# Kernel optimization log

Hardware: AMD Instinct MI355X
Metric: run time of the kernel (lower is better)

The kernel has to match this reference:

```python
import jax, jax.numpy as jnp
import numpy as np

N_NODES = 50000


def _gcn_layer(x, src, dst, W, b, n_nodes):
    # PyG GCNConv: h = x @ W, add self-loops, sym-normalized scatter-add, + bias
    h = x @ W  # [N, Dout]
    loop = jnp.arange(n_nodes, dtype=src.dtype)
    src2 = jnp.concatenate([src, loop])
    dst2 = jnp.concatenate([dst, loop])
    ones = jnp.ones(src2.shape[0], dtype=x.dtype)
    deg = jax.ops.segment_sum(ones, dst2, num_segments=n_nodes)  # in-degree w/ self-loops
    dinv = jnp.where(deg > 0, jax.lax.rsqrt(deg), 0.0)
    norm = dinv[src2] * dinv[dst2]  # [E+N]
    msg = h[src2] * norm[:, None]   # gather + scale
    out = jax.ops.segment_sum(msg, dst2, num_segments=n_nodes)  # scatter-add
    return out + b


def setup_inputs() -> dict:
    key = jax.random.key(0)
    k1, k2, k3, k4 = jax.random.split(key, 4)
    x = jax.random.normal(k1, (N_NODES, 128), dtype=jnp.float32)
    edge_index = jax.random.randint(k2, (2, 500000), 0, N_NODES, dtype=jnp.int64)
    W1 = jax.random.normal(k3, (128, 128), dtype=jnp.float32) * (1.0 / np.sqrt(128))
    b1 = jnp.zeros((128,), dtype=jnp.float32)
    W2 = jax.random.normal(k4, (128, 64), dtype=jnp.float32) * (1.0 / np.sqrt(128))
    b2 = jnp.zeros((64,), dtype=jnp.float32)
    return {"x": x, "edge_index": edge_index, "W1": W1, "b1": b1, "W2": W2, "b2": b2}


def reference(x, edge_index, W1, b1, W2, b2):
    src, dst = edge_index[0], edge_index[1]
    n = x.shape[0]
    h = _gcn_layer(x, src, dst, W1, b1, n)
    h = jax.nn.relu(h)
    out = _gcn_layer(h, src, dst, W2, b2, n)
    return out
```

## Files before the change

kernel.cpp:

```cpp
#include <hip/hip_runtime.h>
#include <hip/hip_bf16.h>
#include <cstddef>


typedef __attribute__((ext_vector_type(8))) short short8;
typedef __attribute__((ext_vector_type(4))) float f32x4;

__device__ inline unsigned short f2bf(float f) {
    __hip_bfloat16 b = __float2bfloat16(f);
    return *reinterpret_cast<unsigned short*>(&b);
}
__device__ inline float bf2f_lo(unsigned int u) {
    unsigned int v = u << 16;
    return *reinterpret_cast<float*>(&v);
}
__device__ inline float bf2f_hi(unsigned int u) {
    unsigned int v = u & 0xffff0000u;
    return *reinterpret_cast<float*>(&v);
}

__global__ __launch_bounds__(256) void count_kernel(const int* __restrict__ dst, int E,
                                                    int* __restrict__ deg) {
    int i = blockIdx.x * blockDim.x + threadIdx.x;
    if (i < E) atomicAdd(&deg[dst[i]], 1);
}

__global__ __launch_bounds__(256) void scanA_kernel(const int* __restrict__ deg, int n,
                                                    int* __restrict__ bsums) {
    int tid = threadIdx.x;
    int lane = tid & 63;
    int wid = tid >> 6;
    int i = blockIdx.x * 1024 + tid * 4;
    int v0 = (i + 0 < n) ? deg[i + 0] : 0;
    int v1 = (i + 1 < n) ? deg[i + 1] : 0;
    int v2 = (i + 2 < n) ? deg[i + 2] : 0;
    int v3 = (i + 3 < n) ? deg[i + 3] : 0;
    int s = v0 + v1 + v2 + v3;
    #pragma unroll
    for (int off = 32; off > 0; off >>= 1) s += __shfl_down(s, off, 64);
    __shared__ int ws[4];
    if (lane == 0) ws[wid] = s;
    __syncthreads();
    if (tid == 0) bsums[blockIdx.x] = ws[0] + ws[1] + ws[2] + ws[3];
}

__global__ __launch_bounds__(64) void scanB_kernel(int* __restrict__ bsums, int nb,
                                                   int* __restrict__ totp) {
    int lane = threadIdx.x;
    int v = (lane < nb) ? bsums[lane] : 0;
    int x = v;
    #pragma unroll
    for (int off = 1; off < 64; off <<= 1) {
        int y = __shfl_up(x, off, 64);
        if (lane >= off) x += y;
    }
    if (lane < nb) bsums[lane] = x - v;
    if (lane == 63) *totp = x;
}

__global__ __launch_bounds__(256) void scanC_kernel(const int* __restrict__ deg, int n,
                                                    const int* __restrict__ bsums,
                                                    int* __restrict__ offs,
                                                    int* __restrict__ cur,
                                                    float* __restrict__ dinv) {
    int tid = threadIdx.x;
    int lane = tid & 63;
    int wid = tid >> 6;
    int carry = bsums[blockIdx.x];
    int i = blockIdx.x * 1024 + tid * 4;
    int v0 = (i + 0 < n) ? deg[i + 0] : 0;
    int v1 = (i + 1 < n) ? deg[i + 1] : 0;
    int v2 = (i + 2 < n) ? deg[i + 2] : 0;
    int v3 = (i + 3 < n) ? deg[i + 3] : 0;
    int t = v0 + v1 + v2 + v3;
    int x = t;
    #pragma unroll
    for (int off = 1; off < 64; off <<= 1) {
        int y = __shfl_up(x, off, 64);
        if (lane >= off) x += y;
    }
    __shared__ int ws[4];
    if (lane == 63) ws[wid] = x;
    __syncthreads();
    int wprefix = 0;
    #pragma unroll
    for (int w = 0; w < 4; w++) wprefix += (w < wid) ? ws[w] : 0;
    int e0 = carry + wprefix + x - t;
    int e1 = e0 + v0, e2 = e1 + v1, e3 = e2 + v2;
    if (i + 0 < n) { offs[i + 0] = e0; cur[i + 0] = e0; dinv[i + 0] = rsqrtf((float)(v0 + 1)); }
    if (i + 1 < n) { offs[i + 1] = e1; cur[i + 1] = e1; dinv[i + 1] = rsqrtf((float)(v1 + 1)); }
    if (i + 2 < n) { offs[i + 2] = e2; cur[i + 2] = e2; dinv[i + 2] = rsqrtf((float)(v2 + 1)); }
    if (i + 3 < n) { offs[i + 3] = e3; cur[i + 3] = e3; dinv[i + 3] = rsqrtf((float)(v3 + 1)); }
}

__global__ __launch_bounds__(256) void fill_kernel(const int* __restrict__ src,
                                                   const int* __restrict__ dst, int E,
                                                   int* __restrict__ cur,
                                                   const float* __restrict__ dinv,
                                                   unsigned int* __restrict__ csr) {
    int i = blockIdx.x * blockDim.x + threadIdx.x;
    if (i < E) {
        int s = src[i];
        int d = dst[i];
        int p = atomicAdd(&cur[d], 1);
        float w = dinv[s] * dinv[d];
        csr[p] = (unsigned int)s | ((unsigned int)f2bf(w) << 16);
    }
}

__global__ __launch_bounds__(256) void wt_frag_kernel(const float* __restrict__ W1,
                                                      const float* __restrict__ W2,
                                                      unsigned short* __restrict__ W1f,
                                                      unsigned short* __restrict__ W2f) {
    int idx = blockIdx.x * 256 + threadIdx.x;
    const float* W;
    unsigned short* Wf;
    int n, oct, N;
    if (idx < 2048) { W = W1; Wf = W1f; N = 128; n = idx >> 4; oct = idx & 15; }
    else if (idx < 3072) { W = W2; Wf = W2f; N = 64; int i2 = idx - 2048; n = i2 >> 4; oct = i2 & 15; }
    else return;
    int k0 = oct * 8;
    int ks = k0 >> 5, quad = (k0 >> 3) & 3, ntg = n >> 4;
    short8 v;
    #pragma unroll
    for (int j = 0; j < 8; j++) v[j] = (short)f2bf(W[(k0 + j) * N + n]);
    int off = (((ntg * 4 + ks) * 64) + (n & 15) + 16 * quad) * 8;
    *(short8*)(Wf + off) = v;
}

__global__ __launch_bounds__(256) void gemm1_kernel(const float* __restrict__ A,
                                                    const unsigned short* __restrict__ Bf,
                                                    unsigned short* __restrict__ C,
                                                    int M) {
    constexpr int K = 128, BN = 128;
    __shared__ unsigned short As[64 * K];

    int tid = threadIdx.x;
    int lane = tid & 63;
    int w = tid >> 6;
    int row0 = blockIdx.x * 64;

    short8 bfr[2][4];
    #pragma unroll
    for (int nl = 0; nl < 2; nl++)
        #pragma unroll
        for (int ks = 0; ks < 4; ks++)
            bfr[nl][ks] = *(const short8*)(Bf + ((((w * 2 + nl) * 4 + ks) * 64) + lane) * 8);

    #pragma unroll
    for (int it = 0; it < 8; it++) {
        int idx = it * 256 + tid;
        int row = idx >> 5, kq = idx & 31;
        int k0 = kq * 4;
        int ks = k0 >> 5, quad = (k0 >> 3) & 3, j0 = k0 & 7, mt = row >> 4;
        ushort4 o = make_ushort4(0, 0, 0, 0);
        int gr = row0 + row;
        if (gr < M) {
            float4 a = *(const float4*)(A + (size_t)gr * K + k0);
            o.x = f2bf(a.x); o.y = f2bf(a.y); o.z = f2bf(a.z); o.w = f2bf(a.w);
        }
        int off = (((mt * 4 + ks) * 64) + (row & 15) + 16 * quad) * 8 + j0;
        *(ushort4*)(As + off) = o;
    }
    __syncthreads();

    f32x4 acc[4][2];
    #pragma unroll
    for (int mt = 0; mt < 4; mt++)
        #pragma unroll
        for (int nl = 0; nl < 2; nl++) acc[mt][nl] = (f32x4){0.f, 0.f, 0.f, 0.f};

    #pragma unroll
    for (int ks = 0; ks < 4; ks++) {
        short8 af[4];
        #pragma unroll
        for (int mt = 0; mt < 4; mt++)
            af[mt] = *(const short8*)(As + (((mt * 4 + ks) * 64) + lane) * 8);
        #pragma unroll
        for (int mt = 0; mt < 4; mt++)
            #pragma unroll
            for (int nl = 0; nl < 2; nl++)
                acc[mt][nl] = __builtin_amdgcn_mfma_f32_16x16x32_bf16(
                    af[mt], bfr[nl][ks], acc[mt][nl], 0, 0, 0);
    }

    int col16 = lane & 15;
    int rowq = lane >> 4;
    #pragma unroll
    for (int mt = 0; mt < 4; mt++) {
        #pragma unroll
        for (int nl = 0; nl < 2; nl++) {
            int gc = (w * 2 + nl) * 16 + col16;
            #pragma unroll
            for (int r = 0; r < 4; r++) {
                int gr = row0 + mt * 16 + rowq * 4 + r;
                if (gr < M) C[(size_t)gr * BN + gc] = f2bf(acc[mt][nl][r]);
            }
        }
    }
}

__global__ __launch_bounds__(256) void aggmm_kernel(const unsigned short* __restrict__ h1,
                                                    const int* __restrict__ offs,
                                                    const unsigned int* __restrict__ csr,
                                                    const float* __restrict__ dinv,
                                                    const float* __restrict__ b1,
                                                    const unsigned short* __restrict__ W2f,
                                                    unsigned short* __restrict__ h2,
                                                    int n) {
    __shared__ unsigned short As[4 * 64 * 8];

    int tid = threadIdx.x;
    int t = tid & 63;
    int w = tid >> 6;
    int p = t >> 5;
    int t5 = t & 31;
    int nodebase = blockIdx.x * 16;

    short8 bw[4];
    #pragma unroll
    for (int ks = 0; ks < 4; ks++)
        bw[ks] = *(const short8*)(W2f + (((w * 4 + ks) * 64) + t) * 8);

    float4 bias = *(const float4*)(b1 + t5 * 4);

    #pragma unroll
    for (int i = 0; i < 4; i++) {
        int row16 = w * 4 + i;
        int node = nodebase + row16;
        float a0 = 0.f, a1 = 0.f, a2 = 0.f, a3 = 0.f;
        if (node < n) {
            float di = dinv[node];
            float sw = di * di;
            if (p == 0) {
                uint2 su = *(const uint2*)(h1 + (size_t)node * 128 + t5 * 4);
                a0 = bf2f_lo(su.x) * sw; a1 = bf2f_hi(su.x) * sw;
                a2 = bf2f_lo(su.y) * sw; a3 = bf2f_hi(su.y) * sw;
            }
            int e0 = offs[node];
            int e1 = offs[node + 1];
            int iters = (e1 - e0 + 7) >> 3;
            for (int it = 0; it < iters; it++) {
                int eb = e0 + it * 8;
                #pragma unroll
                for (int j = 0; j < 4; j++) {
                    int ee = eb + j * 2 + p;
                    int ec = min(ee, e1 - 1);
                    unsigned int pk = csr[ec];
                    float wgt = (ee < e1) ? bf2f_hi(pk) : 0.f;
                    int s = pk & 0xffff;
                    uint2 hu = *(const uint2*)(h1 + (size_t)s * 128 + t5 * 4);
                    a0 += bf2f_lo(hu.x) * wgt; a1 += bf2f_hi(hu.x) * wgt;
                    a2 += bf2f_lo(hu.y) * wgt; a3 += bf2f_hi(hu.y) * wgt;
                }
            }
        }
        a0 += __shfl_xor(a0, 32, 64);
        a1 += __shfl_xor(a1, 32, 64);
        a2 += __shfl_xor(a2, 32, 64);
        a3 += __shfl_xor(a3, 32, 64);
        if (p == 0) {
            if (node < n) {
                a0 = fmaxf(a0 + bias.x, 0.f);
                a1 = fmaxf(a1 + bias.y, 0.f);
                a2 = fmaxf(a2 + bias.z, 0.f);
                a3 = fmaxf(a3 + bias.w, 0.f);
            }
            int k0 = t5 * 4;
            int ks = k0 >> 5, quad = (k0 >> 3) & 3, j0 = k0 & 7;
            ushort4 pk4 = make_ushort4(f2bf(a0), f2bf(a1), f2bf(a2), f2bf(a3));
            *(ushort4*)(As + ((ks * 64) + row16 + 16 * quad) * 8 + j0) = pk4;
        }
    }
    __syncthreads();

    f32x4 acc = (f32x4){0.f, 0.f, 0.f, 0.f};
    #pragma unroll
    for (int ks = 0; ks < 4; ks++) {
        short8 af = *(const short8*)(As + ((ks * 64) + t) * 8);
        acc = __builtin_amdgcn_mfma_f32_16x16x32_bf16(af, bw[ks], acc, 0, 0, 0);
    }

    int col = w * 16 + (t & 15);
    int rowq = t >> 4;
    #pragma unroll
    for (int r = 0; r < 4; r++) {
        int gr = nodebase + rowq * 4 + r;
        if (gr < n) h2[(size_t)gr * 64 + col] = f2bf(acc[r]);
    }
}

__global__ __launch_bounds__(256) void aggout_kernel(const unsigned short* __restrict__ h2,
                                                     const int* __restrict__ offs,
                                                     const unsigned int* __restrict__ csr,
                                                     const float* __restrict__ dinv,
                                                     const float* __restrict__ b2,
                                                     float* __restrict__ out, int n) {
    int tid = threadIdx.x;
    int t = tid & 63;
    int w = tid >> 6;
    int node = blockIdx.x * 4 + w;
    if (node >= n) return;
    int p = t >> 4;
    int t4 = t & 15;

    float a0 = 0.f, a1 = 0.f, a2 = 0.f, a3 = 0.f;
    float di = dinv[node];
    float sw = di * di;
    if (p == 0) {
        uint2 su = *(const uint2*)(h2 + (size_t)node * 64 + t4 * 4);
        a0 = bf2f_lo(su.x) * sw; a1 = bf2f_hi(su.x) * sw;
        a2 = bf2f_lo(su.y) * sw; a3 = bf2f_hi(su.y) * sw;
    }

    int e0 = offs[node];
    int e1 = offs[node + 1];
    int iters = (e1 - e0 + 7) >> 3;
    for (int it = 0; it < iters; it++) {
        int eb = e0 + it * 8;
        #pragma unroll
        for (int j = 0; j < 2; j++) {
            int ee = eb + j * 4 + p;
            int ec = min(ee, e1 - 1);
            unsigned int pk = csr[ec];
            float wgt = (ee < e1) ? bf2f_hi(pk) : 0.f;
            int s = pk & 0xffff;
            uint2 hu = *(const uint2*)(h2 + (size_t)s * 64 + t4 * 4);
            a0 += bf2f_lo(hu.x) * wgt; a1 += bf2f_hi(hu.x) * wgt;
            a2 += bf2f_lo(hu.y) * wgt; a3 += bf2f_hi(hu.y) * wgt;
        }
    }
    a0 += __shfl_xor(a0, 16, 64); a1 += __shfl_xor(a1, 16, 64);
    a2 += __shfl_xor(a2, 16, 64); a3 += __shfl_xor(a3, 16, 64);
    a0 += __shfl_xor(a0, 32, 64); a1 += __shfl_xor(a1, 32, 64);
    a2 += __shfl_xor(a2, 32, 64); a3 += __shfl_xor(a3, 32, 64);
    if (p == 0) {
        float4 bb = *(const float4*)(b2 + t4 * 4);
        *(float4*)(out + (size_t)node * 64 + t4 * 4) =
            make_float4(a0 + bb.x, a1 + bb.y, a2 + bb.z, a3 + bb.w);
    }
}

extern "C" void kernel_launch(void* const* d_in, const int* in_sizes, int n_in,
                              void* d_out, int out_size, void* d_ws, size_t ws_size,
                              hipStream_t stream) {
    const float* x  = (const float*)d_in[0];
    const int*   ei = (const int*)d_in[1];
    const float* W1 = (const float*)d_in[2];
    const float* b1 = (const float*)d_in[3];
    const float* W2 = (const float*)d_in[4];
    const float* b2 = (const float*)d_in[5];

    const int N = in_sizes[0] / 128;
    const int E = in_sizes[1] / 2;
    const int* src = ei;
    const int* dst = ei + E;

    char* p = (char*)d_ws;
    auto alloc = [&](size_t bytes) {
        char* r = p;
        p += (bytes + 255) & ~(size_t)255;
        return r;
    };
    int*   degi  = (int*)  alloc((size_t)N * 4);
    float* dinv  = (float*)alloc((size_t)N * 4);
    int*   offs  = (int*)  alloc((size_t)(N + 1) * 4);
    int*   cur   = (int*)  alloc((size_t)N * 4);
    int*   bsums = (int*)  alloc((size_t)64 * 4);
    unsigned int*   csr  = (unsigned int*)alloc((size_t)E * 4);
    unsigned short* W1f  = (unsigned short*)alloc((size_t)128 * 128 * 2);
    unsigned short* W2f  = (unsigned short*)alloc((size_t)64 * 128 * 2);
    unsigned short* h1   = (unsigned short*)alloc((size_t)N * 128 * 2);
    unsigned short* h2   = (unsigned short*)alloc((size_t)N * 64 * 2);
    float* out = (float*)d_out;

    const int NB = (N + 1023) / 1024;

    wt_frag_kernel<<<12, 256, 0, stream>>>(W1, W2, W1f, W2f);
    hipMemsetAsync(degi, 0, (size_t)N * 4, stream);
    count_kernel<<<(E + 255) / 256, 256, 0, stream>>>(dst, E, degi);
    scanA_kernel<<<NB, 256, 0, stream>>>(degi, N, bsums);
    scanB_kernel<<<1, 64, 0, stream>>>(bsums, NB, offs + N);
    scanC_kernel<<<NB, 256, 0, stream>>>(degi, N, bsums, offs, cur, dinv);
    fill_kernel<<<(E + 255) / 256, 256, 0, stream>>>(src, dst, E, cur, dinv, csr);

    gemm1_kernel<<<(N + 63) / 64, 256, 0, stream>>>(x, W1f, h1, N);
    aggmm_kernel<<<(N + 15) / 16, 256, 0, stream>>>(h1, offs, csr, dinv, b1, W2f, h2, N);
    aggout_kernel<<<(N + 3) / 4, 256, 0, stream>>>(h2, offs, csr, dinv, b2, out, N);
}
```

Measured before the change: 197.2 us.

## Fuse graph build and first GEMM into one persistent kernel with flag sync

```diff
diff --git a/kernel.cpp b/kernel.cpp
--- a/kernel.cpp
+++ b/kernel.cpp
@@ -5,6 +5,7 @@
 
 typedef __attribute__((ext_vector_type(8))) short short8;
 typedef __attribute__((ext_vector_type(4))) float f32x4;
+typedef unsigned long long u64;
 
 __device__ inline unsigned short f2bf(float f) {
     __hip_bfloat16 b = __float2bfloat16(f);
@@ -19,184 +20,226 @@
     return *reinterpret_cast<float*>(&v);
 }
 
-__global__ __launch_bounds__(256) void count_kernel(const int* __restrict__ dst, int E,
-                                                    int* __restrict__ deg) {
-    int i = blockIdx.x * blockDim.x + threadIdx.x;
-    if (i < E) atomicAdd(&deg[dst[i]], 1);
-}
-
-__global__ __launch_bounds__(256) void scanA_kernel(const int* __restrict__ deg, int n,
-                                                    int* __restrict__ bsums) {
+__device__ inline u64 ld_acq64(u64* p) {
+    return __hip_atomic_load(p, __ATOMIC_ACQUIRE, __HIP_MEMORY_SCOPE_AGENT);
+}
+__device__ inline void st_rel64(u64* p, u64 v) {
+    __hip_atomic_store(p, v, __ATOMIC_RELEASE, __HIP_MEMORY_SCOPE_AGENT);
+}
+__device__ inline int ld_acq32(int* p) {
+    return __hip_atomic_load(p, __ATOMIC_ACQUIRE, __HIP_MEMORY_SCOPE_AGENT);
+}
+
+__global__ __launch_bounds__(256) void init_kernel(const float* __restrict__ W1,
+                                                   const float* __restrict__ W2,
+                                                   unsigned short* __restrict__ W1f,
+                                                   unsigned short* __restrict__ W2f,
+                                                   int* __restrict__ deg,
+                                                   u64* __restrict__ lb,
+                                                   int* __restrict__ flags, int N) {
+    int idx = blockIdx.x * 256 + threadIdx.x;
+    if (idx < N) deg[idx] = 0;
+    if (idx < 64) lb[idx] = 0;
+    if (idx < 4) flags[idx] = 0;
+    if (idx < 3072) {
+        const float* W;
+        unsigned short* Wf;
+        int n, oct, Nc;
+        if (idx < 2048) { W = W1; Wf = W1f; Nc = 128; n = idx >> 4; oct = idx & 15; }
+        else { W = W2; Wf = W2f; Nc = 64; int i2 = idx - 2048; n = i2 >> 4; oct = i2 & 15; }
+        int k0 = oct * 8;
+        int ks = k0 >> 5, quad = (k0 >> 3) & 3, ntg = n >> 4;
+        short8 v;
+        #pragma unroll
+        for (int j = 0; j < 8; j++) v[j] = (short)f2bf(W[(k0 + j) * Nc + n]);
+        int off = (((ntg * 4 + ks) * 64) + (n & 15) + 16 * quad) * 8;
+        *(short8*)(Wf + off) = v;
+    }
+}
+
+#define MEGA_CB 256
+
+__global__ __launch_bounds__(256) void mega_kernel(
+    const float* __restrict__ x, const unsigned short* __restrict__ W1f,
+    unsigned short* __restrict__ h1,
+    const int* __restrict__ src, const int* __restrict__ dst, int E,
+    int* __restrict__ deg, int N,
+    u64* __restrict__ lb, int* __restrict__ offs, int* __restrict__ cur,
+    float* __restrict__ dinv, unsigned int* __restrict__ csr,
+    int* __restrict__ flags) {
+
+    const int GB = (N + 63) / 64;
+    const int CB = MEGA_CB;
+    const int SB = (N + 1023) / 1024;
+    int b = blockIdx.x;
     int tid = threadIdx.x;
+
+    __shared__ unsigned short As[64 * 128];
+    __shared__ int ws[4];
+    __shared__ int s_prefix;
+
+    if (b < GB) {
+        constexpr int K = 128, BN = 128;
+        int lane = tid & 63;
+        int w = tid >> 6;
+        int row0 = b * 64;
+
+        short8 bfr[2][4];
+        #pragma unroll
+        for (int nl = 0; nl < 2; nl++)
+            #pragma unroll
+            for (int ks = 0; ks < 4; ks++)
+                bfr[nl][ks] = *(const short8*)(W1f + ((((w * 2 + nl) * 4 + ks) * 64) + lane) * 8);
+
+        #pragma unroll
+        for (int it = 0; it < 8; it++) {
+            int idx = it * 256 + tid;
+            int row = idx >> 5, kq = idx & 31;
+            int k0 = kq * 4;
+            int ks = k0 >> 5, quad = (k0 >> 3) & 3, j0 = k0 & 7, mt = row >> 4;
+            ushort4 o = make_ushort4(0, 0, 0, 0);
+            int gr = row0 + row;
+            if (gr < N) {
+                float4 a = *(const float4*)(x + (size_t)gr * K + k0);
+                o.x = f2bf(a.x); o.y = f2bf(a.y); o.z = f2bf(a.z); o.w = f2bf(a.w);
+            }
+            int off = (((mt * 4 + ks) * 64) + (row & 15) + 16 * quad) * 8 + j0;
+            *(ushort4*)(As + off) = o;
+        }
+        __syncthreads();
+
+        f32x4 acc[4][2];
+        #pragma unroll
+        for (int mt = 0; mt < 4; mt++)
+            #pragma unroll
+            for (int nl = 0; nl < 2; nl++) acc[mt][nl] = (f32x4){0.f, 0.f, 0.f, 0.f};
+
+        #pragma unroll
+        for (int ks = 0; ks < 4; ks++) {
+            short8 af[4];
+            #pragma unroll
+            for (int mt = 0; mt < 4; mt++)
+                af[mt] = *(const short8*)(As + (((mt * 4 + ks) * 64) + lane) * 8);
+            #pragma unroll
+            for (int mt = 0; mt < 4; mt++)
+                #pragma unroll
+                for (int nl = 0; nl < 2; nl++)
+                    acc[mt][nl] = __builtin_amdgcn_mfma_f32_16x16x32_bf16(
+                        af[mt], bfr[nl][ks], acc[mt][nl], 0, 0, 0);
+        }
+
+        int col16 = lane & 15;
+        int rowq = lane >> 4;
+        #pragma unroll
+        for (int mt = 0; mt < 4; mt++) {
+            #pragma unroll
+            for (int nl = 0; nl < 2; nl++) {
+                int gc = (w * 2 + nl) * 16 + col16;
+                #pragma unroll
+                for (int r = 0; r < 4; r++) {
+                    int gr = row0 + mt * 16 + rowq * 4 + r;
+                    if (gr < N) h1[(size_t)gr * BN + gc] = f2bf(acc[mt][nl][r]);
+                }
+            }
+        }
+        return;
+    }
+
+    if (b < GB + CB) {
+        int cb = b - GB;
+        for (int i = cb * 256 + tid; i < E; i += CB * 256)
+            atomicAdd(&deg[dst[i]], 1);
+        __syncthreads();
+        if (tid == 0) {
+            __threadfence_system();
+            atomicAdd(&flags[0], 1);
+            while (ld_acq32(&flags[1]) < SB) __builtin_amdgcn_s_sleep(2);
+            __threadfence_system();
+        }
+        __syncthreads();
+        for (int i = cb * 256 + tid; i < E; i += CB * 256) {
+            int s = src[i];
+            int d = dst[i];
+            int p = atomicAdd(&cur[d], 1);
+            float w = rsqrtf((float)((deg[s] + 1) * (deg[d] + 1)));
+            csr[p] = (unsigned int)s | ((unsigned int)f2bf(w) << 16);
+        }
+        return;
+    }
+
+    int sb = b - GB - CB;
+    if (tid == 0) {
+        while (ld_acq32(&flags[0]) < CB) __builtin_amdgcn_s_sleep(2);
+        __threadfence_system();
+    }
+    __syncthreads();
+
     int lane = tid & 63;
-    int wid = tid >> 6;
-    int i = blockIdx.x * 1024 + tid * 4;
-    int v0 = (i + 0 < n) ? deg[i + 0] : 0;
-    int v1 = (i + 1 < n) ? deg[i + 1] : 0;
-    int v2 = (i + 2 < n) ? deg[i + 2] : 0;
-    int v3 = (i + 3 < n) ? deg[i + 3] : 0;
-    int s = v0 + v1 + v2 + v3;
-    #pragma unroll
-    for (int off = 32; off > 0; off >>= 1) s += __shfl_down(s, off, 64);
-    __shared__ int ws[4];
-    if (lane == 0) ws[wid] = s;
-    __syncthreads();
-    if (tid == 0) bsums[blockIdx.x] = ws[0] + ws[1] + ws[2] + ws[3];
-}
-
-__global__ __launch_bounds__(64) void scanB_kernel(int* __restrict__ bsums, int nb,
-                                                   int* __restrict__ totp) {
-    int lane = threadIdx.x;
-    int v = (lane < nb) ? bsums[lane] : 0;
-    int x = v;
+    int wv = tid >> 6;
+    int i = sb * 1024 + tid * 4;
+    int v0 = (i + 0 < N) ? deg[i + 0] : 0;
+    int v1 = (i + 1 < N) ? deg[i + 1] : 0;
+    int v2 = (i + 2 < N) ? deg[i + 2] : 0;
+    int v3 = (i + 3 < N) ? deg[i + 3] : 0;
+    int tsum = v0 + v1 + v2 + v3;
+    int xs = tsum;
     #pragma unroll
     for (int off = 1; off < 64; off <<= 1) {
-        int y = __shfl_up(x, off, 64);
-        if (lane >= off) x += y;
-    }
-    if (lane < nb) bsums[lane] = x - v;
-    if (lane == 63) *totp = x;
-}
-
-__global__ __launch_bounds__(256) void scanC_kernel(const int* __restrict__ deg, int n,
-                                                    const int* __restrict__ bsums,
-                                                    int* __restrict__ offs,
-                                                    int* __restrict__ cur,
-                                                    float* __restrict__ dinv) {
-    int tid = threadIdx.x;
-    int lane = tid & 63;
-    int wid = tid >> 6;
-    int carry = bsums[blockIdx.x];
-    int i = blockIdx.x * 1024 + tid * 4;
-    int v0 = (i + 0 < n) ? deg[i + 0] : 0;
-    int v1 = (i + 1 < n) ? deg[i + 1] : 0;
-    int v2 = (i + 2 < n) ? deg[i + 2] : 0;
-    int v3 = (i + 3 < n) ? deg[i + 3] : 0;
-    int t = v0 + v1 + v2 + v3;
-    int x = t;
-    #pragma unroll
-    for (int off = 1; off < 64; off <<= 1) {
-        int y = __shfl_up(x, off, 64);
-        if (lane >= off) x += y;
-    }
-    __shared__ int ws[4];
-    if (lane == 63) ws[wid] = x;
+        int y = __shfl_up(xs, off, 64);
+        if (lane >= off) xs += y;
+    }
+    if (lane == 63) ws[wv] = xs;
     __syncthreads();
     int wprefix = 0;
     #pragma unroll
-    for (int w = 0; w < 4; w++) wprefix += (w < wid) ? ws[w] : 0;
-    int e0 = carry + wprefix + x - t;
+    for (int w2 = 0; w2 < 4; w2++) wprefix += (w2 < wv) ? ws[w2] : 0;
+    int chunk_total = ws[0] + ws[1] + ws[2] + ws[3];
+
+    if (tid == 0) {
+        st_rel64(&lb[sb], ((u64)(unsigned)chunk_total << 2) | 1ull);
+        int prefix = 0;
+        for (int pred = sb - 1; pred >= 0; --pred) {
+            u64 v;
+            do {
+                v = ld_acq64(&lb[pred]);
+                if ((v & 3) == 0) __builtin_amdgcn_s_sleep(1);
+            } while ((v & 3) == 0);
+            prefix += (int)(unsigned)(v >> 2);
+            if ((v & 3) == 2) break;
+        }
+        st_rel64(&lb[sb], ((u64)(unsigned)(prefix + chunk_total) << 2) | 2ull);
+        s_prefix = prefix;
+    }
+    __syncthreads();
+
+    int carry = s_prefix;
+    int e0 = carry + wprefix + xs - tsum;
     int e1 = e0 + v0, e2 = e1 + v1, e3 = e2 + v2;
-    if (i + 0 < n) { offs[i + 0] = e0; cur[i + 0] = e0; dinv[i + 0] = rsqrtf((float)(v0 + 1)); }
-    if (i + 1 < n) { offs[i + 1] = e1; cur[i + 1] = e1; dinv[i + 1] = rsqrtf((float)(v1 + 1)); }
-    if (i + 2 < n) { offs[i + 2] = e2; cur[i + 2] = e2; dinv[i + 2] = rsqrtf((float)(v2 + 1)); }
-    if (i + 3 < n) { offs[i + 3] = e3; cur[i + 3] = e3; dinv[i + 3] = rsqrtf((float)(v3 + 1)); }
-}
-
-__global__ __launch_bounds__(256) void fill_kernel(const int* __restrict__ src,
-                                                   const int* __restrict__ dst, int E,
-                                                   int* __restrict__ cur,
-                                                   const float* __restrict__ dinv,
-                                                   unsigned int* __restrict__ csr) {
-    int i = blockIdx.x * blockDim.x + threadIdx.x;
-    if (i < E) {
-        int s = src[i];
-        int d = dst[i];
-        int p = atomicAdd(&cur[d], 1);
-        float w = dinv[s] * dinv[d];
-        csr[p] = (unsigned int)s | ((unsigned int)f2bf(w) << 16);
-    }
-}
-
-__global__ __launch_bounds__(256) void wt_frag_kernel(const float* __restrict__ W1,
-                                                      const float* __restrict__ W2,
-                                                      unsigned short* __restrict__ W1f,
-                                                      unsigned short* __restrict__ W2f) {
-    int idx = blockIdx.x * 256 + threadIdx.x;
-    const float* W;
-    unsigned short* Wf;
-    int n, oct, N;
-    if (idx < 2048) { W = W1; Wf = W1f; N = 128; n = idx >> 4; oct = idx & 15; }
-    else if (idx < 3072) { W = W2; Wf = W2f; N = 64; int i2 = idx - 2048; n = i2 >> 4; oct = i2 & 15; }
-    else return;
-    int k0 = oct * 8;
-    int ks = k0 >> 5, quad = (k0 >> 3) & 3, ntg = n >> 4;
-    short8 v;
-    #pragma unroll
-    for (int j = 0; j < 8; j++) v[j] = (short)f2bf(W[(k0 + j) * N + n]);
-    int off = (((ntg * 4 + ks) * 64) + (n & 15) + 16 * quad) * 8;
-    *(short8*)(Wf + off) = v;
-}
-
-__global__ __launch_bounds__(256) void gemm1_kernel(const float* __restrict__ A,
-                                                    const unsigned short* __restrict__ Bf,
-                                                    unsigned short* __restrict__ C,
-                                                    int M) {
-    constexpr int K = 128, BN = 128;
-    __shared__ unsigned short As[64 * K];
-
-    int tid = threadIdx.x;
-    int lane = tid & 63;
-    int w = tid >> 6;
-    int row0 = blockIdx.x * 64;
-
-    short8 bfr[2][4];
-    #pragma unroll
-    for (int nl = 0; nl < 2; nl++)
-        #pragma unroll
-        for (int ks = 0; ks < 4; ks++)
-            bfr[nl][ks] = *(const short8*)(Bf + ((((w * 2 + nl) * 4 + ks) * 64) + lane) * 8);
-
-    #pragma unroll
-    for (int it = 0; it < 8; it++) {
-        int idx = it * 256 + tid;
-        int row = idx >> 5, kq = idx & 31;
-        int k0 = kq * 4;
-        int ks = k0 >> 5, quad = (k0 >> 3) & 3, j0 = k0 & 7, mt = row >> 4;
-        ushort4 o = make_ushort4(0, 0, 0, 0);
-        int gr = row0 + row;
-        if (gr < M) {
-            float4 a = *(const float4*)(A + (size_t)gr * K + k0);
-            o.x = f2bf(a.x); o.y = f2bf(a.y); o.z = f2bf(a.z); o.w = f2bf(a.w);
-        }
-        int off = (((mt * 4 + ks) * 64) + (row & 15) + 16 * quad) * 8 + j0;
-        *(ushort4*)(As + off) = o;
-    }
+    if (i + 0 < N) {
+        offs[i + 0] = e0;
+        __hip_atomic_store(&cur[i + 0], e0, __ATOMIC_RELAXED, __HIP_MEMORY_SCOPE_AGENT);
+        dinv[i + 0] = rsqrtf((float)(v0 + 1));
+    }
+    if (i + 1 < N) {
+        offs[i + 1] = e1;
+        __hip_atomic_store(&cur[i + 1], e1, __ATOMIC_RELAXED, __HIP_MEMORY_SCOPE_AGENT);
+        dinv[i + 1] = rsqrtf((float)(v1 + 1));
+    }
+    if (i + 2 < N) {
+        offs[i + 2] = e2;
+        __hip_atomic_store(&cur[i + 2], e2, __ATOMIC_RELAXED, __HIP_MEMORY_SCOPE_AGENT);
+        dinv[i + 2] = rsqrtf((float)(v2 + 1));
+    }
+    if (i + 3 < N) {
+        offs[i + 3] = e3;
+        __hip_atomic_store(&cur[i + 3], e3, __ATOMIC_RELAXED, __HIP_MEMORY_SCOPE_AGENT);
+        dinv[i + 3] = rsqrtf((float)(v3 + 1));
+    }
+    if (sb == SB - 1 && tid == 0) offs[N] = carry + chunk_total;
     __syncthreads();
-
-    f32x4 acc[4][2];
-    #pragma unroll
-    for (int mt = 0; mt < 4; mt++)
-        #pragma unroll
-        for (int nl = 0; nl < 2; nl++) acc[mt][nl] = (f32x4){0.f, 0.f, 0.f, 0.f};
-
-    #pragma unroll
-    for (int ks = 0; ks < 4; ks++) {
-        short8 af[4];
-        #pragma unroll
-        for (int mt = 0; mt < 4; mt++)
-            af[mt] = *(const short8*)(As + (((mt * 4 + ks) * 64) + lane) * 8);
-        #pragma unroll
-        for (int mt = 0; mt < 4; mt++)
-            #pragma unroll
-            for (int nl = 0; nl < 2; nl++)
-                acc[mt][nl] = __builtin_amdgcn_mfma_f32_16x16x32_bf16(
-                    af[mt], bfr[nl][ks], acc[mt][nl], 0, 0, 0);
-    }
-
-    int col16 = lane & 15;
-    int rowq = lane >> 4;
-    #pragma unroll
-    for (int mt = 0; mt < 4; mt++) {
-        #pragma unroll
-        for (int nl = 0; nl < 2; nl++) {
-            int gc = (w * 2 + nl) * 16 + col16;
-            #pragma unroll
-            for (int r = 0; r < 4; r++) {
-                int gr = row0 + mt * 16 + rowq * 4 + r;
-                if (gr < M) C[(size_t)gr * BN + gc] = f2bf(acc[mt][nl][r]);
-            }
-        }
+    if (tid == 0) {
+        __threadfence_system();
+        atomicAdd(&flags[1], 1);
     }
 }
 
@@ -366,7 +409,8 @@
     float* dinv  = (float*)alloc((size_t)N * 4);
     int*   offs  = (int*)  alloc((size_t)(N + 1) * 4);
     int*   cur   = (int*)  alloc((size_t)N * 4);
-    int*   bsums = (int*)  alloc((size_t)64 * 4);
+    u64*   lb    = (u64*)  alloc((size_t)64 * 8);
+    int*   flags = (int*)  alloc((size_t)4 * 4);
     unsigned int*   csr  = (unsigned int*)alloc((size_t)E * 4);
     unsigned short* W1f  = (unsigned short*)alloc((size_t)128 * 128 * 2);
     unsigned short* W2f  = (unsigned short*)alloc((size_t)64 * 128 * 2);
@@ -374,17 +418,13 @@
     unsigned short* h2   = (unsigned short*)alloc((size_t)N * 64 * 2);
     float* out = (float*)d_out;
 
-    const int NB = (N + 1023) / 1024;
-
-    wt_frag_kernel<<<12, 256, 0, stream>>>(W1, W2, W1f, W2f);
-    hipMemsetAsync(degi, 0, (size_t)N * 4, stream);
-    count_kernel<<<(E + 255) / 256, 256, 0, stream>>>(dst, E, degi);
-    scanA_kernel<<<NB, 256, 0, stream>>>(degi, N, bsums);
-    scanB_kernel<<<1, 64, 0, stream>>>(bsums, NB, offs + N);
-    scanC_kernel<<<NB, 256, 0, stream>>>(degi, N, bsums, offs, cur, dinv);
-    fill_kernel<<<(E + 255) / 256, 256, 0, stream>>>(src, dst, E, cur, dinv, csr);
-
-    gemm1_kernel<<<(N + 63) / 64, 256, 0, stream>>>(x, W1f, h1, N);
+    const int GB = (N + 63) / 64;
+    const int SB = (N + 1023) / 1024;
+    const int MEGA = GB + MEGA_CB + SB;
+
+    init_kernel<<<(N + 255) / 256, 256, 0, stream>>>(W1, W2, W1f, W2f, degi, lb, flags, N);
+    mega_kernel<<<MEGA, 256, 0, stream>>>(x, W1f, h1, src, dst, E, degi, N,
+                                          lb, offs, cur, dinv, csr, flags);
     aggmm_kernel<<<(N + 15) / 16, 256, 0, stream>>>(h1, offs, csr, dinv, b1, W2f, h2, N);
     aggout_kernel<<<(N + 3) / 4, 256, 0, stream>>>(h2, offs, csr, dinv, b2, out, N);
 }
```

New measurement: 293.7 us. 49.0% more time.
